# Kernel tuning notes

Measured on AMD Instinct MI355X. Metric: run time of the kernel, lower is better.

Reference implementation:

```python
import jax, jax.numpy as jnp
import numpy as np

WIN = 8
SHIFT = WIN // 2  # shift=True
NH = 12
HD = 32
EPS = 1e-5


def _rel_pos_index(w):
    coords = np.stack(np.meshgrid(np.arange(w), np.arange(w), indexing='ij')).reshape(2, -1)
    rel = (coords[:, :, None] - coords[:, None, :]).transpose(1, 2, 0)
    rel[..., 0] += w - 1
    rel[..., 1] += w - 1
    rel[..., 0] *= 2 * w - 1
    return rel.sum(-1)  # [w*w, w*w]

REL_IDX = jnp.asarray(_rel_pos_index(WIN), dtype=jnp.int32)


def _ln(x, g, b):
    mu = jnp.mean(x, axis=-1, keepdims=True)
    var = jnp.mean(jnp.square(x - mu), axis=-1, keepdims=True)
    return (x - mu) * jax.lax.rsqrt(var + EPS) * g + b


def setup_inputs() -> dict:
    key = jax.random.key(0)
    ks = jax.random.split(key, 8)
    B, Hh, Ww, C = 16, 64, 64, 384
    s = lambda fan: 1.0 / np.sqrt(fan)
    return {
        'x': jax.random.normal(ks[0], (B, Hh * Ww, C), jnp.float32),
        'norm1_g': jnp.ones((C,), jnp.float32),
        'norm1_b': jnp.zeros((C,), jnp.float32),
        'qkv_w': jax.random.normal(ks[1], (3 * C, C), jnp.float32) * s(C),
        'qkv_b': jnp.zeros((3 * C,), jnp.float32),
        'proj_w': jax.random.normal(ks[2], (C, C), jnp.float32) * s(C),
        'proj_b': jnp.zeros((C,), jnp.float32),
        'rpb_table': jax.random.normal(ks[3], ((2 * WIN - 1) ** 2, NH), jnp.float32) * 0.02,
        'norm2_g': jnp.ones((C,), jnp.float32),
        'norm2_b': jnp.zeros((C,), jnp.float32),
        'fc1_w': jax.random.normal(ks[4], (4 * C, C), jnp.float32) * s(C),
        'fc1_b': jnp.zeros((4 * C,), jnp.float32),
        'fc2_w': jax.random.normal(ks[5], (C, 4 * C), jnp.float32) * s(4 * C),
        'fc2_b': jnp.zeros((C,), jnp.float32),
        'H': Hh,
        'W': Ww,
    }


def reference(x, norm1_g, norm1_b, qkv_w, qkv_b, proj_w, proj_b, rpb_table,
              norm2_g, norm2_b, fc1_w, fc1_b, fc2_w, fc2_b, H, W):
    B, N, C = x.shape
    Nw = WIN * WIN
    shortcut = x
    h = _ln(x, norm1_g, norm1_b)

    # window partition with roll (shifted windows)
    h = h.reshape(B, H, W, C)
    h = jnp.roll(h, shift=(-SHIFT, -SHIFT), axis=(1, 2))
    h = h.reshape(B, H // WIN, WIN, W // WIN, WIN, C).transpose(0, 1, 3, 2, 4, 5)
    h = h.reshape(-1, Nw, C)  # [B*nW, 64, C]

    # window attention
    qkv = h @ qkv_w.T + qkv_b  # [Bw, Nw, 3C]
    qkv = qkv.reshape(-1, Nw, 3, NH, HD).transpose(2, 0, 3, 1, 4)
    q, k, v = qkv[0], qkv[1], qkv[2]  # [Bw, NH, Nw, HD]
    attn = jnp.einsum('bhqd,bhkd->bhqk', q, k) * (HD ** -0.5)
    bias = rpb_table[REL_IDX.reshape(-1)].reshape(Nw, Nw, NH).transpose(2, 0, 1)
    attn = jax.nn.softmax(attn + bias[None], axis=-1)
    o = jnp.einsum('bhqk,bhkd->bhqd', attn, v)
    o = o.transpose(0, 2, 1, 3).reshape(-1, Nw, C)
    o = o @ proj_w.T + proj_b

    # window reverse with inverse roll
    o = o.reshape(B, H // WIN, W // WIN, WIN, WIN, C).transpose(0, 1, 3, 2, 4, 5)
    o = o.reshape(B, H, W, C)
    o = jnp.roll(o, shift=(SHIFT, SHIFT), axis=(1, 2)).reshape(B, N, C)

    x = shortcut + o
    m = _ln(x, norm2_g, norm2_b)
    m = jax.nn.gelu(m @ fc1_w.T + fc1_b, approximate=False)
    m = m @ fc2_w.T + fc2_b
    return x + m
```

## Files before the change

### kernel.cpp

```cpp
#include <hip/hip_runtime.h>
#include <hip/hip_bf16.h>
#include <math.h>

typedef __attribute__((ext_vector_type(8))) short bf16x8;
typedef __attribute__((ext_vector_type(4))) float f32x4;
typedef unsigned short u16;

#define NHEAD 12

__device__ __forceinline__ u16 f2bf(float f) {
  unsigned int u = __builtin_bit_cast(unsigned int, f);
  return (u16)((u + 0x7fffu + ((u >> 16) & 1u)) >> 16);
}

__device__ __forceinline__ void gload16(const void* g, void* l) {
  __builtin_amdgcn_global_load_lds(
      (const __attribute__((address_space(1))) void*)g,
      (__attribute__((address_space(3))) void*)l, 16, 0, 0);
}

__global__ void cvt_all(const float* __restrict__ s0, const float* __restrict__ s1,
                        const float* __restrict__ s2, const float* __restrict__ s3,
                        u16* __restrict__ d) {
  int i = blockIdx.x * 256 + threadIdx.x;
  if (i >= 1769472) return;
  float v;
  if (i < 442368) v = s0[i];
  else if (i < 589824) v = s1[i - 442368];
  else if (i < 1179648) v = s2[i - 589824];
  else v = s3[i - 1179648];
  d[i] = f2bf(v);
}

__global__ void build_bias(const float* __restrict__ rpb, float* __restrict__ bt) {
  int i = blockIdx.x * 256 + threadIdx.x;
  if (i >= NHEAD * 4096) return;
  int h = i >> 12;
  int q = (i >> 6) & 63;
  int k = i & 63;
  int qi = q >> 3, qj = q & 7, ki = k >> 3, kj = k & 7;
  int idx = (qi - ki + 7) * 15 + (qj - kj + 7);
  bt[i] = rpb[idx * NHEAD + h];
}

__global__ __launch_bounds__(256) void ln_k(const float* __restrict__ x,
                                            const float* __restrict__ g,
                                            const float* __restrict__ b,
                                            u16* __restrict__ out) {
  int row = (blockIdx.x << 2) + (threadIdx.x >> 6);
  int lane = threadIdx.x & 63;
  const float* xr = x + (size_t)row * 384;
  float v[6];
  float s = 0.f;
#pragma unroll
  for (int i = 0; i < 6; ++i) { v[i] = xr[lane + (i << 6)]; s += v[i]; }
#pragma unroll
  for (int o = 32; o; o >>= 1) s += __shfl_xor(s, o, 64);
  float mu = s * (1.f / 384.f);
  float vs = 0.f;
#pragma unroll
  for (int i = 0; i < 6; ++i) { float d0 = v[i] - mu; vs += d0 * d0; }
#pragma unroll
  for (int o = 32; o; o >>= 1) vs += __shfl_xor(vs, o, 64);
  float rs = rsqrtf(vs * (1.f / 384.f) + 1e-5f);
  u16* orow = out + (size_t)row * 384;
#pragma unroll
  for (int i = 0; i < 6; ++i) {
    int c = lane + (i << 6);
    orow[c] = f2bf((v[i] - mu) * rs * g[c] + b[c]);
  }
}

template <int EP>
__global__ __launch_bounds__(512, 4) void gemm8(const u16* __restrict__ A,
                                                const u16* __restrict__ W,
                                                const float* __restrict__ bias,
                                                const float* __restrict__ res,
                                                void* __restrict__ outp,
                                                int N, int K, int nCol) {
  __shared__ u16 As[3][256 * 32];
  __shared__ u16 Bs[3][128 * 32];
  const int tid = threadIdx.x;
  const int wave = tid >> 6, lane = tid & 63;
  const int wm = wave >> 1, wn = wave & 1;
  const int nwg = gridDim.x;
  const int cpx = nwg >> 3;
  const int lin = (blockIdx.x & 7) * cpx + (blockIdx.x >> 3);
  const int rowT = lin / nCol;
  const int colT = lin - rowT * nCol;
  const int rowBase = rowT << 8;
  const int colBase = colT << 7;
  const int nK = K >> 5;

  const int srow = tid >> 2;
  const int scb = (tid & 3) ^ ((tid >> 3) & 3);
  const u16* Asrc = A + (size_t)(rowBase + srow) * K + (scb << 3);
  const u16* Wsrc = W + (size_t)(colBase + srow) * K + (scb << 3);
  const int ldst = tid << 3;

  auto stage = [&](int j_, int b_) {
    const size_t k0_ = (size_t)(j_ << 5);
    gload16(Asrc + k0_, &As[b_][ldst]);
    gload16(Asrc + (size_t)128 * K + k0_, &As[b_][4096 + ldst]);
    gload16(Wsrc + k0_, &Bs[b_][ldst]);
  };

  const int slot8 = (((lane >> 4) ^ ((lane >> 1) & 3)) << 3);
  const int arow0 = (wm << 6) + (lane & 15);
  const int brow0 = (wn << 6) + (lane & 15);

  f32x4 acc[4][4] = {};

  stage(0, 0);
  stage(1, 1);
  int bj = 0, bs = 2;
  for (int j = 0; j < nK; ++j) {
    if (j < nK - 1) asm volatile("s_waitcnt vmcnt(3)" ::: "memory");
    else            asm volatile("s_waitcnt vmcnt(0)" ::: "memory");
    __builtin_amdgcn_sched_barrier(0);
    __builtin_amdgcn_s_barrier();
    __builtin_amdgcn_sched_barrier(0);
    if (j + 2 < nK) stage(j + 2, bs);
    const u16* ab = As[bj];
    const u16* bb = Bs[bj];
    bf16x8 aF[4], bF[2];
#pragma unroll
    for (int m = 0; m < 4; ++m)
      aF[m] = *(const bf16x8*)&ab[(arow0 + (m << 4)) * 32 + slot8];
#pragma unroll
    for (int n = 0; n < 2; ++n)
      bF[n] = *(const bf16x8*)&bb[(brow0 + (n << 4)) * 32 + slot8];
    __builtin_amdgcn_s_setprio(1);
#pragma unroll
    for (int m = 0; m < 4; ++m)
#pragma unroll
      for (int n = 0; n < 2; ++n)
        acc[m][n] = __builtin_amdgcn_mfma_f32_16x16x32_bf16(aF[m], bF[n], acc[m][n], 0, 0, 0);
    __builtin_amdgcn_s_setprio(0);
#pragma unroll
    for (int n = 0; n < 2; ++n)
      bF[n] = *(const bf16x8*)&bb[(brow0 + ((n + 2) << 4)) * 32 + slot8];
    __builtin_amdgcn_s_setprio(1);
#pragma unroll
    for (int m = 0; m < 4; ++m)
#pragma unroll
      for (int n = 0; n < 2; ++n)
        acc[m][n + 2] = __builtin_amdgcn_mfma_f32_16x16x32_bf16(aF[m], bF[n], acc[m][n + 2], 0, 0, 0);
    __builtin_amdgcn_s_setprio(0);
    __builtin_amdgcn_sched_barrier(0);
    bj = (bj == 2) ? 0 : bj + 1;
    bs = (bs == 2) ? 0 : bs + 1;
  }

#pragma unroll
  for (int m = 0; m < 4; ++m) {
#pragma unroll
    for (int n = 0; n < 4; ++n) {
      const int col = colBase + (wn << 6) + (n << 4) + (lane & 15);
      const int row0 = rowBase + (wm << 6) + (m << 4) + ((lane >> 4) << 2);
      const float bv = bias[col];
#pragma unroll
      for (int jj = 0; jj < 4; ++jj) {
        const size_t row = (size_t)(row0 + jj);
        float y = acc[m][n][jj] + bv;
        if (EP == 0) {
          ((u16*)outp)[row * N + col] = f2bf(y);
        } else if (EP == 1) {
          ((float*)outp)[row * N + col] = y + res[row * N + col];
        } else if (EP == 2) {
          float u = 0.7978845608028654f * (y + 0.044715f * y * y * y);
          float t = 1.f - 2.f / (1.f + __expf(2.f * u));
          y = 0.5f * y * (1.f + t);
          ((u16*)outp)[row * N + col] = f2bf(y);
        } else {
          ((float*)outp)[row * N + col] = y + res[row * N + col];
        }
      }
    }
  }
}

__global__ __launch_bounds__(256) void attn_k(const u16* __restrict__ qkv,
                                              const float* __restrict__ bias_tab,
                                              u16* __restrict__ o) {
  const int cpx = gridDim.x >> 3;
  const int lin = (blockIdx.x & 7) * cpx + (blockIdx.x >> 3);
  const int w = lin / NHEAD;
  const int h = lin - w * NHEAD;
  const int tid = threadIdx.x, wave = tid >> 6, lane = tid & 63;
  __shared__ u16 q_s[64 * 32];
  __shared__ u16 k_s[64 * 32];
  __shared__ u16 vt_s[32 * 64];
  __shared__ u16 p_s[4][16 * 72];
  const int b = w >> 6;
  const int wim = w & 63;
  const int wr0 = (wim >> 3) << 3, wc0 = (wim & 7) << 3;
  {
    const int r = tid >> 2, d0 = (tid & 3) << 3;
    const int pr = r >> 3, pc = r & 7;
    const int orow = (wr0 + pr + 4) & 63, ocol = (wc0 + pc + 4) & 63;
    const size_t t = ((size_t)b << 12) + (orow << 6) + ocol;
    const u16* base = qkv + t * 1152 + h * 32 + d0;
    *(uint4*)&q_s[r * 32 + d0] = *(const uint4*)(base);
    *(uint4*)&k_s[r * 32 + d0] = *(const uint4*)(base + 384);
    u16 vv[8];
    *(uint4*)vv = *(const uint4*)(base + 768);
#pragma unroll
    for (int j = 0; j < 8; ++j) vt_s[(d0 + j) * 64 + r] = vv[j];
  }
  __syncthreads();
  const int cIdx = lane & 15, rgrp = lane >> 4;
  const f32x4 zz = {0.f, 0.f, 0.f, 0.f};
  bf16x8 qa = *(const bf16x8*)&q_s[((wave << 4) + cIdx) * 32 + (rgrp << 3)];
  f32x4 s_acc[4];
#pragma unroll
  for (int n = 0; n < 4; ++n) {
    bf16x8 kb = *(const bf16x8*)&k_s[((n << 4) + cIdx) * 32 + (rgrp << 3)];
    s_acc[n] = __builtin_amdgcn_mfma_f32_16x16x32_bf16(qa, kb, zz, 0, 0, 0);
  }
  const float scale = 0.1767766952966369f;
  float mrow[4] = {-1e30f, -1e30f, -1e30f, -1e30f};
  const float* bt = bias_tab + h * 4096 + ((wave << 4) + (rgrp << 2)) * 64 + cIdx;
#pragma unroll
  for (int n = 0; n < 4; ++n)
#pragma unroll
    for (int j = 0; j < 4; ++j) {
      float val = s_acc[n][j] * scale + bt[j * 64 + (n << 4)];
      s_acc[n][j] = val;
      mrow[j] = fmaxf(mrow[j], val);
    }
#pragma unroll
  for (int j = 0; j < 4; ++j)
#pragma unroll
    for (int o2 = 1; o2 < 16; o2 <<= 1) mrow[j] = fmaxf(mrow[j], __shfl_xor(mrow[j], o2, 64));
  float srow[4] = {0.f, 0.f, 0.f, 0.f};
#pragma unroll
  for (int n = 0; n < 4; ++n)
#pragma unroll
    for (int j = 0; j < 4; ++j) {
      float e = __expf(s_acc[n][j] - mrow[j]);
      s_acc[n][j] = e;
      srow[j] += e;
    }
#pragma unroll
  for (int j = 0; j < 4; ++j)
#pragma unroll
    for (int o2 = 1; o2 < 16; o2 <<= 1) srow[j] += __shfl_xor(srow[j], o2, 64);
  float rinv[4];
#pragma unroll
  for (int j = 0; j < 4; ++j) rinv[j] = 1.f / srow[j];
  u16* pw = p_s[wave];
#pragma unroll
  for (int n = 0; n < 4; ++n)
#pragma unroll
    for (int j = 0; j < 4; ++j)
      pw[((rgrp << 2) + j) * 72 + (n << 4) + cIdx] = f2bf(s_acc[n][j] * rinv[j]);
  f32x4 o_acc[2] = {};
#pragma unroll
  for (int kk = 0; kk < 2; ++kk) {
    bf16x8 pa = *(const bf16x8*)&pw[cIdx * 72 + (kk << 5) + (rgrp << 3)];
#pragma unroll
    for (int c2 = 0; c2 < 2; ++c2) {
      bf16x8 vb = *(const bf16x8*)&vt_s[((c2 << 4) + cIdx) * 64 + (kk << 5) + (rgrp << 3)];
      o_acc[c2] = __builtin_amdgcn_mfma_f32_16x16x32_bf16(pa, vb, o_acc[c2], 0, 0, 0);
    }
  }
#pragma unroll
  for (int c2 = 0; c2 < 2; ++c2)
#pragma unroll
    for (int j = 0; j < 4; ++j) {
      const int p = (wave << 4) + (rgrp << 2) + j;
      const int pr = p >> 3, pc = p & 7;
      const int orow = (wr0 + pr + 4) & 63, ocol = (wc0 + pc + 4) & 63;
      const size_t t = ((size_t)b << 12) + (orow << 6) + ocol;
      o[t * 384 + h * 32 + (c2 << 4) + cIdx] = f2bf(o_acc[c2][j]);
    }
}

extern "C" void kernel_launch(void* const* d_in, const int* in_sizes, int n_in,
                              void* d_out, int out_size, void* d_ws, size_t ws_size,
                              hipStream_t stream) {
  const float* x = (const float*)d_in[0];
  const float* n1g = (const float*)d_in[1];
  const float* n1b = (const float*)d_in[2];
  const float* qkv_w = (const float*)d_in[3];
  const float* qkv_b = (const float*)d_in[4];
  const float* proj_w = (const float*)d_in[5];
  const float* proj_b = (const float*)d_in[6];
  const float* rpb = (const float*)d_in[7];
  const float* n2g = (const float*)d_in[8];
  const float* n2b = (const float*)d_in[9];
  const float* fc1_w = (const float*)d_in[10];
  const float* fc1_b = (const float*)d_in[11];
  const float* fc2_w = (const float*)d_in[12];
  const float* fc2_b = (const float*)d_in[13];

  char* ws = (char*)d_ws;
  u16* wqkv = (u16*)(ws + 0);
  u16* wproj = (u16*)(ws + 884736);
  u16* wfc1 = (u16*)(ws + 1179648);
  u16* wfc2 = (u16*)(ws + 2359296);
  float* bias_tab = (float*)(ws + 3538944);
  u16* qkv = (u16*)(ws + 3735552);
  u16* m1 = qkv;
  u16* hbuf = (u16*)(ws + 205062144);
  u16* obuf = hbuf;
  float* x1 = (float*)d_out;

  cvt_all<<<(1769472 + 255) / 256, 256, 0, stream>>>(qkv_w, proj_w, fc1_w, fc2_w, wqkv);
  build_bias<<<192, 256, 0, stream>>>(rpb, bias_tab);

  ln_k<<<16384, 256, 0, stream>>>(x, n1g, n1b, hbuf);
  gemm8<0><<<2304, 512, 0, stream>>>(hbuf, wqkv, qkv_b, nullptr, qkv, 1152, 384, 9);
  attn_k<<<12288, 256, 0, stream>>>(qkv, bias_tab, obuf);
  gemm8<1><<<768, 512, 0, stream>>>(obuf, wproj, proj_b, x, x1, 384, 384, 3);
  ln_k<<<16384, 256, 0, stream>>>(x1, n2g, n2b, hbuf);
  gemm8<2><<<3072, 512, 0, stream>>>(hbuf, wfc1, fc1_b, nullptr, m1, 1536, 384, 12);
  gemm8<3><<<768, 512, 0, stream>>>(m1, wfc2, fc2_b, x1, (float*)d_out, 384, 1536, 3);
}
```

Before: 547.3 us.

## Replace pipelined 256x128 GEMM with simpler 128x128 BK64 single-buffer kernel

Rewrites the shared GEMM kernel to use 128x128 output tiles with 256 threads, a K-step of 64 and a single LDS buffer per operand, using a new XOR swizzle. It removes the triple-buffered async prefetch, manual waitcnt and priority hints in favour of plain __syncthreads around each stage. The aim is higher occupancy and a simpler schedule with more blocks, at the cost of losing load/compute overlap and halving A-tile reuse per block.

```diff
diff --git a/kernel.cpp b/kernel.cpp
--- a/kernel.cpp
+++ b/kernel.cpp
@@ -72,84 +72,62 @@
 }
 
 template <int EP>
-__global__ __launch_bounds__(512, 4) void gemm8(const u16* __restrict__ A,
+__global__ __launch_bounds__(256, 3) void gemmA(const u16* __restrict__ A,
                                                 const u16* __restrict__ W,
                                                 const float* __restrict__ bias,
                                                 const float* __restrict__ res,
                                                 void* __restrict__ outp,
                                                 int N, int K, int nCol) {
-  __shared__ u16 As[3][256 * 32];
-  __shared__ u16 Bs[3][128 * 32];
+  __shared__ u16 As[128 * 64];
+  __shared__ u16 Bs[128 * 64];
   const int tid = threadIdx.x;
   const int wave = tid >> 6, lane = tid & 63;
   const int wm = wave >> 1, wn = wave & 1;
-  const int nwg = gridDim.x;
-  const int cpx = nwg >> 3;
+  const int nwg = gridDim.x, cpx = nwg >> 3;
   const int lin = (blockIdx.x & 7) * cpx + (blockIdx.x >> 3);
   const int rowT = lin / nCol;
   const int colT = lin - rowT * nCol;
-  const int rowBase = rowT << 8;
+  const int rowBase = rowT << 7;
   const int colBase = colT << 7;
-  const int nK = K >> 5;
-
-  const int srow = tid >> 2;
-  const int scb = (tid & 3) ^ ((tid >> 3) & 3);
-  const u16* Asrc = A + (size_t)(rowBase + srow) * K + (scb << 3);
-  const u16* Wsrc = W + (size_t)(colBase + srow) * K + (scb << 3);
+  const int nK = K >> 6;
+
+  const int g16 = (tid & 7) ^ ((tid >> 3) & 7);
+  const u16* Asrc = A + (size_t)(rowBase + (tid >> 3)) * K + (g16 << 3);
+  const u16* Wsrc = W + (size_t)(colBase + (tid >> 3)) * K + (g16 << 3);
   const int ldst = tid << 3;
 
-  auto stage = [&](int j_, int b_) {
-    const size_t k0_ = (size_t)(j_ << 5);
-    gload16(Asrc + k0_, &As[b_][ldst]);
-    gload16(Asrc + (size_t)128 * K + k0_, &As[b_][4096 + ldst]);
-    gload16(Wsrc + k0_, &Bs[b_][ldst]);
-  };
-
-  const int slot8 = (((lane >> 4) ^ ((lane >> 1) & 3)) << 3);
-  const int arow0 = (wm << 6) + (lane & 15);
-  const int brow0 = (wn << 6) + (lane & 15);
+  const int q4 = lane >> 4;
+  const int rx = lane & 7;
+  const int arow = (wm << 6) + (lane & 15);
+  const int brow = (wn << 6) + (lane & 15);
 
   f32x4 acc[4][4] = {};
 
-  stage(0, 0);
-  stage(1, 1);
-  int bj = 0, bs = 2;
   for (int j = 0; j < nK; ++j) {
-    if (j < nK - 1) asm volatile("s_waitcnt vmcnt(3)" ::: "memory");
-    else            asm volatile("s_waitcnt vmcnt(0)" ::: "memory");
-    __builtin_amdgcn_sched_barrier(0);
-    __builtin_amdgcn_s_barrier();
-    __builtin_amdgcn_sched_barrier(0);
-    if (j + 2 < nK) stage(j + 2, bs);
-    const u16* ab = As[bj];
-    const u16* bb = Bs[bj];
-    bf16x8 aF[4], bF[2];
-#pragma unroll
-    for (int m = 0; m < 4; ++m)
-      aF[m] = *(const bf16x8*)&ab[(arow0 + (m << 4)) * 32 + slot8];
-#pragma unroll
-    for (int n = 0; n < 2; ++n)
-      bF[n] = *(const bf16x8*)&bb[(brow0 + (n << 4)) * 32 + slot8];
-    __builtin_amdgcn_s_setprio(1);
-#pragma unroll
-    for (int m = 0; m < 4; ++m)
-#pragma unroll
-      for (int n = 0; n < 2; ++n)
-        acc[m][n] = __builtin_amdgcn_mfma_f32_16x16x32_bf16(aF[m], bF[n], acc[m][n], 0, 0, 0);
-    __builtin_amdgcn_s_setprio(0);
-#pragma unroll
-    for (int n = 0; n < 2; ++n)
-      bF[n] = *(const bf16x8*)&bb[(brow0 + ((n + 2) << 4)) * 32 + slot8];
-    __builtin_amdgcn_s_setprio(1);
-#pragma unroll
-    for (int m = 0; m < 4; ++m)
-#pragma unroll
-      for (int n = 0; n < 2; ++n)
-        acc[m][n + 2] = __builtin_amdgcn_mfma_f32_16x16x32_bf16(aF[m], bF[n], acc[m][n + 2], 0, 0, 0);
-    __builtin_amdgcn_s_setprio(0);
-    __builtin_amdgcn_sched_barrier(0);
-    bj = (bj == 2) ? 0 : bj + 1;
-    bs = (bs == 2) ? 0 : bs + 1;
+    const size_t k0 = (size_t)j << 6;
+#pragma unroll
+    for (int c = 0; c < 4; ++c) {
+      gload16(Asrc + (size_t)(c << 5) * K + k0, &As[(c << 11) + ldst]);
+      gload16(Wsrc + (size_t)(c << 5) * K + k0, &Bs[(c << 11) + ldst]);
+    }
+    __syncthreads();
+#pragma unroll
+    for (int kk = 0; kk < 2; ++kk) {
+      const int slot = (((kk << 2) + q4) ^ rx) << 3;
+      bf16x8 aF[4], bF[4];
+#pragma unroll
+      for (int m = 0; m < 4; ++m)
+        aF[m] = *(const bf16x8*)&As[(arow + (m << 4)) * 64 + slot];
+#pragma unroll
+      for (int n = 0; n < 4; ++n)
+        bF[n] = *(const bf16x8*)&Bs[(brow + (n << 4)) * 64 + slot];
+#pragma unroll
+      for (int m = 0; m < 4; ++m)
+#pragma unroll
+        for (int n = 0; n < 4; ++n)
+          acc[m][n] = __builtin_amdgcn_mfma_f32_16x16x32_bf16(aF[m], bF[n], acc[m][n], 0, 0, 0);
+    }
+    __syncthreads();
   }
 
 #pragma unroll
@@ -311,10 +289,10 @@
   build_bias<<<192, 256, 0, stream>>>(rpb, bias_tab);
 
   ln_k<<<16384, 256, 0, stream>>>(x, n1g, n1b, hbuf);
-  gemm8<0><<<2304, 512, 0, stream>>>(hbuf, wqkv, qkv_b, nullptr, qkv, 1152, 384, 9);
+  gemmA<0><<<4608, 256, 0, stream>>>(hbuf, wqkv, qkv_b, nullptr, qkv, 1152, 384, 9);
   attn_k<<<12288, 256, 0, stream>>>(qkv, bias_tab, obuf);
-  gemm8<1><<<768, 512, 0, stream>>>(obuf, wproj, proj_b, x, x1, 384, 384, 3);
+  gemmA<1><<<1536, 256, 0, stream>>>(obuf, wproj, proj_b, x, x1, 384, 384, 3);
   ln_k<<<16384, 256, 0, stream>>>(x1, n2g, n2b, hbuf);
-  gemm8<2><<<3072, 512, 0, stream>>>(hbuf, wfc1, fc1_b, nullptr, m1, 1536, 384, 12);
-  gemm8<3><<<768, 512, 0, stream>>>(m1, wfc2, fc2_b, x1, (float*)d_out, 384, 1536, 3);
-}
+  gemmA<2><<<6144, 256, 0, stream>>>(hbuf, wfc1, fc1_b, nullptr, m1, 1536, 384, 12);
+  gemmA<3><<<1536, 256, 0, stream>>>(m1, wfc2, fc2_b, x1, (float*)d_out, 384, 1536, 3);
+}
```

After: 507.5 us. -7.3%, faster.
